# Kernel tuning notes

Hardware: AMD Instinct MI355X
Metric: run time of the kernel (lower is better)

The kernel has to match this reference:

```python
import jax, jax.numpy as jnp
import numpy as np

DIM_IN, DIM_K, DIM_V = 1024, 1024, 1024

def setup_inputs() -> dict:
    key = jax.random.key(0)
    k1, k2, k3, k4 = jax.random.split(key, 4)
    x = jax.random.normal(k1, (4, 2048, DIM_IN), dtype=jnp.float32)
    # Linear(dim_in, dim_k, bias=False): store as [in, out] for x @ W
    Wq = jax.random.normal(k2, (DIM_IN, DIM_K), dtype=jnp.float32) * (1.0 / np.sqrt(DIM_IN))
    Wk = jax.random.normal(k3, (DIM_IN, DIM_K), dtype=jnp.float32) * (1.0 / np.sqrt(DIM_IN))
    Wv = jax.random.normal(k4, (DIM_IN, DIM_V), dtype=jnp.float32) * (1.0 / np.sqrt(DIM_IN))
    return {"x": x, "Wq": Wq, "Wk": Wk, "Wv": Wv, "causal_mask": 1}

def reference(x, Wq, Wk, Wv, causal_mask):
    # x: [b, n, dim_in]
    b, n, _ = x.shape
    q = jnp.einsum('bnd,dk->bnk', x, Wq)
    k = jnp.einsum('bnd,dk->bnk', x, Wk)
    v = jnp.einsum('bnd,dv->bnv', x, Wv)
    scale = 1.0 / np.sqrt(Wq.shape[1])
    dist = jnp.einsum('bik,bjk->bij', q, k) * scale  # [b, n, n]
    if causal_mask:
        mask = jnp.tril(jnp.ones((n, n), dtype=bool))
        dist = jnp.where(mask, dist, -jnp.inf)
    attn = jax.nn.softmax(dist, axis=-1)
    return jnp.einsum('bij,bjv->biv', attn, v)  # [b, n, dim_v]
```

## Files before the change

kernel.cpp:

```cpp
#include <hip/hip_runtime.h>
#include <hip/hip_bf16.h>
#include <stdint.h>

#define BM 128
#define BN 128
#define BK 64

typedef __attribute__((ext_vector_type(8))) short bf16x8;
typedef __attribute__((ext_vector_type(4))) float floatx4;


__device__ __forceinline__ unsigned short f2bf(float f) {
    unsigned int x;
    __builtin_memcpy(&x, &f, 4);
    unsigned int r = (x + 0x7fffu + ((x >> 16) & 1u)) >> 16;
    return (unsigned short)r;
}

__device__ __forceinline__ float bf2f_hi(unsigned int u_hi_masked) {
    float f;
    __builtin_memcpy(&f, &u_hi_masked, 4);
    return f;
}

__device__ __forceinline__ void async_copy16(const void* g, void* l) {
    __builtin_amdgcn_global_load_lds(
        (const __attribute__((address_space(1))) void*)(uintptr_t)g,
        (__attribute__((address_space(3))) void*)(uint32_t)(uintptr_t)l,
        16, 0, 0);
}


__global__ __launch_bounds__(256) void prep(const float* __restrict__ x,
                                            const float* __restrict__ Wq,
                                            const float* __restrict__ Wk,
                                            const float* __restrict__ Wv,
                                            unsigned short* __restrict__ xb,
                                            unsigned short* __restrict__ wT) {
    __shared__ float tile[32][33];
    int bid = blockIdx.x;
    int tid = threadIdx.x;
    if (bid < 8192) {
        int i = bid * 256 + tid;
        float4 v = ((const float4*)x)[i];
        ushort4 o;
        o.x = f2bf(v.x);
        o.y = f2bf(v.y);
        o.z = f2bf(v.z);
        o.w = f2bf(v.w);
        ((ushort4*)xb)[i] = o;
    } else {
        int w = bid - 8192;
        int z = w >> 10;
        int r = w & 1023;
        int bx = (r & 31) * 32;
        int by = (r >> 5) * 32;
        const float* W = z == 0 ? Wq : (z == 1 ? Wk : Wv);
        int tx = tid & 31, ty = tid >> 5;
        for (int rr = 0; rr < 32; rr += 8)
            tile[ty + rr][tx] = W[(size_t)(by + ty + rr) * 1024 + bx + tx];
        __syncthreads();
        unsigned short* o = wT + (size_t)z * 1024 * 1024;
        for (int rr = 0; rr < 32; rr += 8)
            o[(size_t)(bx + ty + rr) * 1024 + by + tx] = f2bf(tile[tx][ty + rr]);
    }
}


__device__ __forceinline__ void gemm_core(const unsigned short* __restrict__ A,
                                          int lda,
                                          const unsigned short* __restrict__ B,
                                          int ldb, void* __restrict__ C,
                                          int ldc, bool out_bf16, int kend,
                                          float scale, int m0, int n0) {
    __shared__ __align__(16) unsigned short As[BM * BK];
    __shared__ __align__(16) unsigned short Bs[BN * BK];

    int tid = threadIdx.x;
    int lane = tid & 63;
    int wave = tid >> 6;
    int wm = (wave >> 1) * 64;
    int wn = (wave & 1) * 64;
    int fr = lane & 15;
    int kq = lane >> 4;

    floatx4 acc[4][4] = {};

    for (int k0 = 0; k0 < kend; k0 += BK) {
#pragma unroll
        for (int q = 0; q < 4; q++) {
            int c = tid + q * 256;
            int r = c >> 3, ko = (c & 7) * 8;
            async_copy16(A + (size_t)(m0 + r) * lda + k0 + ko, &As[c * 8]);
            async_copy16(B + (size_t)(n0 + r) * ldb + k0 + ko, &Bs[c * 8]);
        }
        __syncthreads();

#pragma unroll
        for (int kh = 0; kh < 2; kh++) {
            int kc = kh * 4 + kq;
            bf16x8 af[4], bfg[4];
#pragma unroll
            for (int mi = 0; mi < 4; mi++)
                af[mi] = *(const bf16x8*)&As[(wm + mi * 16 + fr) * BK + kc * 8];
#pragma unroll
            for (int ni = 0; ni < 4; ni++)
                bfg[ni] = *(const bf16x8*)&Bs[(wn + ni * 16 + fr) * BK + kc * 8];
#pragma unroll
            for (int mi = 0; mi < 4; mi++)
#pragma unroll
                for (int ni = 0; ni < 4; ni++)
                    acc[mi][ni] = __builtin_amdgcn_mfma_f32_16x16x32_bf16(
                        af[mi], bfg[ni], acc[mi][ni], 0, 0, 0);
        }
        __syncthreads();
    }

    int col0 = n0 + wn + fr;
    int rbase = m0 + wm + kq * 4;
    if (out_bf16) {
        unsigned short* Cb = (unsigned short*)C;
#pragma unroll
        for (int mi = 0; mi < 4; mi++)
#pragma unroll
            for (int ni = 0; ni < 4; ni++)
#pragma unroll
                for (int r = 0; r < 4; r++)
                    Cb[(size_t)(rbase + mi * 16 + r) * ldc + col0 + ni * 16] =
                        f2bf(acc[mi][ni][r] * scale);
    } else {
        float* Cb = (float*)C;
#pragma unroll
        for (int mi = 0; mi < 4; mi++)
#pragma unroll
            for (int ni = 0; ni < 4; ni++)
#pragma unroll
                for (int r = 0; r < 4; r++)
                    Cb[(size_t)(rbase + mi * 16 + r) * ldc + col0 + ni * 16] =
                        acc[mi][ni][r] * scale;
    }
}


__global__ __launch_bounds__(256, 4) void gemm_qk(
    const unsigned short* __restrict__ xb, const unsigned short* __restrict__ wT,
    unsigned short* __restrict__ qk) {
    gemm_core(xb, 1024, wT, 1024, qk, 2048, true, 1024, 1.0f,
              blockIdx.y * BM, blockIdx.x * BN);
}


__global__ __launch_bounds__(256, 4) void gemm_s_vt(
    const unsigned short* __restrict__ qk, const unsigned short* __restrict__ wTv,
    const unsigned short* __restrict__ xb, unsigned short* __restrict__ S,
    unsigned short* __restrict__ vt) {
    int bid = blockIdx.x;
    if (bid < 1024) {
        int bz = bid >> 8;
        int r = bid & 255;
        int m0 = (r >> 4) * BM;
        int n0 = (r & 15) * BN;
        if (n0 > m0 + (BM - 1)) return;
        const unsigned short* Q = qk + (size_t)bz * 2048 * 2048;
        const unsigned short* K = qk + (size_t)bz * 2048 * 2048 + 1024;
        unsigned short* Sb = S + (size_t)bz * 2048 * 2048;
        gemm_core(Q, 2048, K, 2048, Sb, 2048, true, 1024, 0.03125f, m0, n0);
    } else {
        int r = bid - 1024;
        int m0 = (r >> 6) * BM;
        int n0 = (r & 63) * BN;
        gemm_core(wTv, 1024, xb, 1024, vt, 8192, true, 1024, 1.0f, m0, n0);
    }
}


__global__ __launch_bounds__(256, 4) void gemm_pv(
    const unsigned short* __restrict__ S, const unsigned short* __restrict__ vt,
    float* __restrict__ out) {
    int bz = blockIdx.z;
    int mb = gridDim.y - 1 - blockIdx.y;
    int m0 = mb * BM;
    int kend = m0 + BM < 2048 ? m0 + BM : 2048;
    gemm_core(S + (size_t)bz * 2048 * 2048, 2048, vt + (size_t)bz * 2048, 8192,
              out + (size_t)bz * 2048 * 1024, 1024, false, kend, 1.0f, m0,
              blockIdx.x * BN);
}


__global__ __launch_bounds__(256) void softmax_causal(unsigned short* __restrict__ S) {
    int wave = threadIdx.x >> 6;
    int lane = threadIdx.x & 63;
    int row = blockIdx.x * 4 + wave;
    int i = row & 2047;
    unsigned short* s = S + (size_t)row * 2048;

    uint4 raw[4];
#pragma unroll
    for (int c = 0; c < 4; c++) raw[c] = ((const uint4*)s)[lane + c * 64];

    const float NEG = -1.0e30f;
    float p[32];
    float m = NEG;
#pragma unroll
    for (int c = 0; c < 4; c++) {
        const unsigned int* u = (const unsigned int*)&raw[c];
#pragma unroll
        for (int w = 0; w < 4; w++) {
            int j = c * 512 + lane * 8 + w * 2;
            float f0 = bf2f_hi(u[w] << 16);
            float f1 = bf2f_hi(u[w] & 0xffff0000u);
            f0 = (j <= i) ? f0 : NEG;
            f1 = (j + 1 <= i) ? f1 : NEG;
            p[c * 8 + w * 2] = f0;
            p[c * 8 + w * 2 + 1] = f1;
            m = fmaxf(m, fmaxf(f0, f1));
        }
    }
#pragma unroll
    for (int o = 32; o > 0; o >>= 1) m = fmaxf(m, __shfl_xor(m, o));

    float sum = 0.f;
#pragma unroll
    for (int t = 0; t < 32; t++) {
        p[t] = __expf(p[t] - m);
        sum += p[t];
    }
#pragma unroll
    for (int o = 32; o > 0; o >>= 1) sum += __shfl_xor(sum, o);
    float inv = 1.0f / sum;

#pragma unroll
    for (int c = 0; c < 4; c++) {
        uint4 out;
        unsigned int* u = (unsigned int*)&out;
#pragma unroll
        for (int w = 0; w < 4; w++) {
            unsigned int lo = f2bf(p[c * 8 + w * 2] * inv);
            unsigned int hi = f2bf(p[c * 8 + w * 2 + 1] * inv);
            u[w] = lo | (hi << 16);
        }
        ((uint4*)s)[lane + c * 64] = out;
    }
}


extern "C" void kernel_launch(void* const* d_in, const int* in_sizes, int n_in,
                              void* d_out, int out_size, void* d_ws,
                              size_t ws_size, hipStream_t stream) {
    const float* x = (const float*)d_in[0];
    const float* Wq = (const float*)d_in[1];
    const float* Wk = (const float*)d_in[2];
    const float* Wv = (const float*)d_in[3];

    char* ws = (char*)d_ws;
    unsigned short* qk = (unsigned short*)(ws);
    unsigned short* S = (unsigned short*)(ws + 33554432);
    unsigned short* vt = (unsigned short*)(ws + 67108864);
    unsigned short* xb = (unsigned short*)(ws + 83886080);
    unsigned short* wT = (unsigned short*)(ws + 100663296);

    prep<<<11264, 256, 0, stream>>>(x, Wq, Wk, Wv, xb, wT);
    gemm_qk<<<dim3(16, 64), 256, 0, stream>>>(xb, wT, qk);
    gemm_s_vt<<<1536, 256, 0, stream>>>(qk, wT + 2 * 1024 * 1024, xb, S, vt);
    softmax_causal<<<2048, 256, 0, stream>>>(S);
    gemm_pv<<<dim3(8, 16, 4), 256, 0, stream>>>(S, vt, (float*)d_out);
}
```

Measured before the change: 260.8 us.

## Launch only causal S tiles and overlap V-transpose GEMM with softmax

The S GEMM now launches exactly the 136 lower-triangular tiles per batch, using a triangular index decode, instead of 256 blocks where half exit early. The V^T projection GEMM moves out of the S kernel into a combined kernel with the softmax, so the compute-bound GEMM blocks run alongside the memory-bound softmax rows. The kernel count stays the same. The risks are that the S GEMM alone may underfill the device, and that mixing heterogeneous blocks could unbalance scheduling.

```diff
diff --git a/kernel.cpp b/kernel.cpp
--- a/kernel.cpp
+++ b/kernel.cpp
@@ -150,26 +150,84 @@
 }
 
 
-__global__ __launch_bounds__(256, 4) void gemm_s_vt(
-    const unsigned short* __restrict__ qk, const unsigned short* __restrict__ wTv,
-    const unsigned short* __restrict__ xb, unsigned short* __restrict__ S,
-    unsigned short* __restrict__ vt) {
+__global__ __launch_bounds__(256, 4) void gemm_s(
+    const unsigned short* __restrict__ qk, unsigned short* __restrict__ S) {
     int bid = blockIdx.x;
-    if (bid < 1024) {
-        int bz = bid >> 8;
-        int r = bid & 255;
-        int m0 = (r >> 4) * BM;
-        int n0 = (r & 15) * BN;
-        if (n0 > m0 + (BM - 1)) return;
-        const unsigned short* Q = qk + (size_t)bz * 2048 * 2048;
-        const unsigned short* K = qk + (size_t)bz * 2048 * 2048 + 1024;
-        unsigned short* Sb = S + (size_t)bz * 2048 * 2048;
-        gemm_core(Q, 2048, K, 2048, Sb, 2048, true, 1024, 0.03125f, m0, n0);
-    } else {
-        int r = bid - 1024;
-        int m0 = (r >> 6) * BM;
-        int n0 = (r & 63) * BN;
-        gemm_core(wTv, 1024, xb, 1024, vt, 8192, true, 1024, 1.0f, m0, n0);
+    int bz = bid / 136;
+    int r = bid - bz * 136;
+    int mb = (int)((sqrtf(8.0f * r + 1.0f) - 1.0f) * 0.5f);
+    while ((mb + 1) * (mb + 2) / 2 <= r) mb++;
+    while (mb * (mb + 1) / 2 > r) mb--;
+    int nb = r - mb * (mb + 1) / 2;
+    const unsigned short* Q = qk + (size_t)bz * 2048 * 2048;
+    const unsigned short* K = Q + 1024;
+    unsigned short* Sb = S + (size_t)bz * 2048 * 2048;
+    gemm_core(Q, 2048, K, 2048, Sb, 2048, true, 1024, 0.03125f, mb * BM,
+              nb * BN);
+}
+
+
+__global__ __launch_bounds__(256, 4) void sm_vt(
+    unsigned short* __restrict__ S, const unsigned short* __restrict__ wTv,
+    const unsigned short* __restrict__ xb, unsigned short* __restrict__ vt) {
+    int bid = blockIdx.x;
+    if (bid < 512) {
+        gemm_core(wTv, 1024, xb, 1024, vt, 8192, true, 1024, 1.0f,
+                  (bid >> 6) * BM, (bid & 63) * BN);
+        return;
+    }
+    int wave = threadIdx.x >> 6;
+    int lane = threadIdx.x & 63;
+    int row = (bid - 512) * 4 + wave;
+    int i = row & 2047;
+    unsigned short* s = S + (size_t)row * 2048;
+
+    uint4 raw[4];
+#pragma unroll
+    for (int c = 0; c < 4; c++) raw[c] = ((const uint4*)s)[lane + c * 64];
+
+    const float NEG = -1.0e30f;
+    float p[32];
+    float m = NEG;
+#pragma unroll
+    for (int c = 0; c < 4; c++) {
+        const unsigned int* u = (const unsigned int*)&raw[c];
+#pragma unroll
+        for (int w = 0; w < 4; w++) {
+            int j = c * 512 + lane * 8 + w * 2;
+            float f0 = bf2f_hi(u[w] << 16);
+            float f1 = bf2f_hi(u[w] & 0xffff0000u);
+            f0 = (j <= i) ? f0 : NEG;
+            f1 = (j + 1 <= i) ? f1 : NEG;
+            p[c * 8 + w * 2] = f0;
+            p[c * 8 + w * 2 + 1] = f1;
+            m = fmaxf(m, fmaxf(f0, f1));
+        }
+    }
+#pragma unroll
+    for (int o = 32; o > 0; o >>= 1) m = fmaxf(m, __shfl_xor(m, o));
+
+    float sum = 0.f;
+#pragma unroll
+    for (int t = 0; t < 32; t++) {
+        p[t] = __expf(p[t] - m);
+        sum += p[t];
+    }
+#pragma unroll
+    for (int o = 32; o > 0; o >>= 1) sum += __shfl_xor(sum, o);
+    float inv = 1.0f / sum;
+
+#pragma unroll
+    for (int c = 0; c < 4; c++) {
+        uint4 out;
+        unsigned int* u = (unsigned int*)&out;
+#pragma unroll
+        for (int w = 0; w < 4; w++) {
+            unsigned int lo = f2bf(p[c * 8 + w * 2] * inv);
+            unsigned int hi = f2bf(p[c * 8 + w * 2 + 1] * inv);
+            u[w] = lo | (hi << 16);
+        }
+        ((uint4*)s)[lane + c * 64] = out;
     }
 }
 
@@ -187,63 +245,6 @@
 }
 
 
-__global__ __launch_bounds__(256) void softmax_causal(unsigned short* __restrict__ S) {
-    int wave = threadIdx.x >> 6;
-    int lane = threadIdx.x & 63;
-    int row = blockIdx.x * 4 + wave;
-    int i = row & 2047;
-    unsigned short* s = S + (size_t)row * 2048;
-
-    uint4 raw[4];
-#pragma unroll
-    for (int c = 0; c < 4; c++) raw[c] = ((const uint4*)s)[lane + c * 64];
-
-    const float NEG = -1.0e30f;
-    float p[32];
-    float m = NEG;
-#pragma unroll
-    for (int c = 0; c < 4; c++) {
-        const unsigned int* u = (const unsigned int*)&raw[c];
-#pragma unroll
-        for (int w = 0; w < 4; w++) {
-            int j = c * 512 + lane * 8 + w * 2;
-            float f0 = bf2f_hi(u[w] << 16);
-            float f1 = bf2f_hi(u[w] & 0xffff0000u);
-            f0 = (j <= i) ? f0 : NEG;
-            f1 = (j + 1 <= i) ? f1 : NEG;
-            p[c * 8 + w * 2] = f0;
-            p[c * 8 + w * 2 + 1] = f1;
-            m = fmaxf(m, fmaxf(f0, f1));
-        }
-    }
-#pragma unroll
-    for (int o = 32; o > 0; o >>= 1) m = fmaxf(m, __shfl_xor(m, o));
-
-    float sum = 0.f;
-#pragma unroll
-    for (int t = 0; t < 32; t++) {
-        p[t] = __expf(p[t] - m);
-        sum += p[t];
-    }
-#pragma unroll
-    for (int o = 32; o > 0; o >>= 1) sum += __shfl_xor(sum, o);
-    float inv = 1.0f / sum;
-
-#pragma unroll
-    for (int c = 0; c < 4; c++) {
-        uint4 out;
-        unsigned int* u = (unsigned int*)&out;
-#pragma unroll
-        for (int w = 0; w < 4; w++) {
-            unsigned int lo = f2bf(p[c * 8 + w * 2] * inv);
-            unsigned int hi = f2bf(p[c * 8 + w * 2 + 1] * inv);
-            u[w] = lo | (hi << 16);
-        }
-        ((uint4*)s)[lane + c * 64] = out;
-    }
-}
-
-
 extern "C" void kernel_launch(void* const* d_in, const int* in_sizes, int n_in,
                               void* d_out, int out_size, void* d_ws,
                               size_t ws_size, hipStream_t stream) {
@@ -261,7 +262,7 @@
 
     prep<<<11264, 256, 0, stream>>>(x, Wq, Wk, Wv, xb, wT);
     gemm_qk<<<dim3(16, 64), 256, 0, stream>>>(xb, wT, qk);
-    gemm_s_vt<<<1536, 256, 0, stream>>>(qk, wT + 2 * 1024 * 1024, xb, S, vt);
-    softmax_causal<<<2048, 256, 0, stream>>>(S);
+    gemm_s<<<544, 256, 0, stream>>>(qk, S);
+    sm_vt<<<2560, 256, 0, stream>>>(S, wT + 2 * 1024 * 1024, xb, vt);
     gemm_pv<<<dim3(8, 16, 4), 256, 0, stream>>>(S, vt, (float*)d_out);
 }
```

Measured after the change: 255.3 us. 2.1% less time.
